# Kernel tuning notes

Hardware: AMD Instinct MI355X
Metric: run time of the kernel (lower is better)

## Reference

```python
import jax, jax.numpy as jnp
import numpy as np

V = 32          # num_variables
T = 48          # num_time_bins
D = 512         # d_model
H = 8           # num_heads
HD = D // H     # head_dim = 64
OD = 16         # observation_dim
B = 4


def setup_inputs() -> dict:
    key = jax.random.key(0)
    ks = jax.random.split(key, 20)
    s = 0.02
    inp = {
        'h': jax.random.normal(ks[0], (B, T, V, D), jnp.float32),
        'observation_state': jax.random.normal(ks[1], (B, T, V, 2), jnp.float32),
        'Wq': jax.random.normal(ks[2], (D, D), jnp.float32) * s,
        'bq': jnp.zeros((D,), jnp.float32),
        'Wk': jax.random.normal(ks[3], (D, D), jnp.float32) * s,
        'bk': jnp.zeros((D,), jnp.float32),
        'Wv': jax.random.normal(ks[4], (D, D), jnp.float32) * s,
        'bv': jnp.zeros((D,), jnp.float32),
        'Wo': jax.random.normal(ks[5], (D, D), jnp.float32) * s,
        'bo': jnp.zeros((D,), jnp.float32),
        'Woq': jax.random.normal(ks[6], (2, H * OD), jnp.float32) * 0.5,
        'boq': jnp.zeros((H * OD,), jnp.float32),
        'Wok': jax.random.normal(ks[7], (2, H * OD), jnp.float32) * 0.5,
        'bok': jnp.zeros((H * OD,), jnp.float32),
        'variable_bias': jax.random.normal(ks[8], (H, V, V), jnp.float32) * 0.01,
        'relative_time_bias': jax.random.normal(ks[9], (H, 2 * T - 1), jnp.float32) * 0.01,
    }
    return inp


def reference(h, observation_state, Wq, bq, Wk, bk, Wv, bv, Wo, bo,
              Woq, boq, Wok, bok, variable_bias, relative_time_bias):
    N = T * V
    scale = 1.0 / np.sqrt(HD)
    obs_scale = 1.0 / np.sqrt(OD)

    # static index buffers (constants)
    flat_var_ids = jnp.tile(jnp.arange(V), T)                       # [N]
    flat_time_ids = jnp.repeat(jnp.arange(T), V)                    # [N]
    rel_index = flat_time_ids[:, None] - flat_time_ids[None, :] + (T - 1)  # [N,N]

    fh = h.reshape(B, N, D)
    fo = observation_state.reshape(B, N, 2)

    def heads(x, nh, hd):
        return x.reshape(B, N, nh, hd).transpose(0, 2, 1, 3)  # [B,H,N,hd]

    q = heads(fh @ Wq + bq, H, HD)
    k = heads(fh @ Wk + bk, H, HD)
    v = heads(fh @ Wv + bv, H, HD)
    oq = heads(fo @ Woq + boq, H, OD)
    ok = heads(fo @ Wok + bok, H, OD)

    content = jnp.einsum('bhnd,bhmd->bhnm', q, k) * scale
    obs = jnp.einsum('bhnd,bhmd->bhnm', oq, ok) * obs_scale
    var_scores = variable_bias[:, flat_var_ids[:, None], flat_var_ids[None, :]]  # [H,N,N]
    time_scores = relative_time_bias[:, rel_index]                                # [H,N,N]

    scores = content + obs + var_scores[None] + time_scores[None]
    attn = jax.nn.softmax(scores, axis=-1)  # dropout off (inference)
    out = jnp.einsum('bhnm,bhmd->bhnd', attn, v)
    out = out.transpose(0, 2, 1, 3).reshape(B, N, D)
    out = out @ Wo + bo
    return out.reshape(B, T, V, D)
```

## Files before the change

### kernel.cpp

```cpp
#include <hip/hip_runtime.h>
#include <math.h>

typedef __bf16 bf16x8 __attribute__((ext_vector_type(8)));
typedef float f32x4 __attribute__((ext_vector_type(4)));

#define NB 4
#define NT 48
#define NV 32
#define ND 512
#define NH 8
#define NN 1536
#define NBN 6144
#define L2E 1.44269504f

#define GLOAD_LDS(g, l) \
    __builtin_amdgcn_global_load_lds( \
        (const __attribute__((address_space(1))) void*)(g), \
        (__attribute__((address_space(3))) void*)(l), 16, 0, 0)

__global__ __launch_bounds__(256) void prep(
    const float* __restrict__ h, const float* __restrict__ obs,
    const float* __restrict__ Wq, const float* __restrict__ Wk,
    const float* __restrict__ Wv, const float* __restrict__ Wo,
    const float* __restrict__ bq, const float* __restrict__ bk,
    const float* __restrict__ bv,
    const float* __restrict__ Wok, const float* __restrict__ bok,
    __bf16* __restrict__ h_bf, __bf16* __restrict__ WcatT,
    __bf16* __restrict__ WoT, float* __restrict__ biascat,
    __bf16* __restrict__ kx)
{
    __shared__ float ts[64][68];
    const int tid = threadIdx.x;
    const int bx = blockIdx.x;
    if (bx < 1536) {
        int t = bx * 256 + tid;
        const float4* src = (const float4*)h + (size_t)t * 2;
        float4 a = src[0], b = src[1];
        __bf16 r[8] = {(__bf16)a.x, (__bf16)a.y, (__bf16)a.z, (__bf16)a.w,
                       (__bf16)b.x, (__bf16)b.y, (__bf16)b.z, (__bf16)b.w};
        *(uint4*)(h_bf + (size_t)t * 8) = *(uint4*)r;
    } else if (bx < 1792) {
        int bw = bx - 1536;
        const int p = bw >> 6, tile = bw & 63;
        const int k0 = (tile >> 3) * 64, c0 = (tile & 7) * 64;
        const float* W = (p == 0) ? Wq : (p == 1) ? Wk : (p == 2) ? Wv : Wo;
        const float scale = (p == 0) ? 0.125f * L2E : 1.0f;
        #pragma unroll
        for (int i = 0; i < 4; i++) {
            int r = (tid >> 4) + i * 16;
            float4 v = *(const float4*)(W + (size_t)(k0 + r) * 512 + c0 + (tid & 15) * 4);
            *(float4*)&ts[r][(tid & 15) * 4] = v;
        }
        __syncthreads();
        __bf16 tmp[16];
        #pragma unroll
        for (int j = 0; j < 16; j++)
            tmp[j] = (__bf16)(ts[(tid & 3) * 16 + j][tid >> 2] * scale);
        int crow = c0 + (tid >> 2);
        __bf16* dst = (p < 3)
            ? WcatT + ((size_t)(p * 512 + crow)) * 512 + k0 + (tid & 3) * 16
            : WoT   + ((size_t)crow) * 512 + k0 + (tid & 3) * 16;
        *(uint4*)dst = *(uint4*)tmp;
        *(uint4*)(dst + 8) = *(uint4*)(tmp + 8);
        if (p < 3 && k0 == 0 && tid < 64) {
            const float* bb = (p == 0) ? bq : (p == 1) ? bk : bv;
            biascat[p * 512 + c0 + tid] = bb[c0 + tid] * scale;
        }
    } else {
        int t = (bx - 1792) * 256 + tid;
        int row = t >> 1, half = t & 1;
        __bf16* dst = kx + (size_t)row * 96 + 64 + half * 16;
        if (half == 0) {
            int bh = row / NN, n = row - bh * NN;
            int b = bh >> 3, hh = bh & 7;
            size_t bn = (size_t)b * NN + n;
            float o0 = obs[bn * 2], o1 = obs[bn * 2 + 1];
            int f = hh * 16;
            __bf16 tmp[16];
            #pragma unroll
            for (int j = 0; j < 16; j++)
                tmp[j] = (__bf16)(o0 * Wok[f + j] + o1 * Wok[128 + f + j] + bok[f + j]);
            *(uint4*)dst       = *(uint4*)tmp;
            *(uint4*)(dst + 8) = *(uint4*)(tmp + 8);
        } else {
            uint4 z = {0, 0, 0, 0};
            *(uint4*)dst       = z;
            *(uint4*)(dst + 8) = z;
        }
    }
}

__global__ __launch_bounds__(256) void kvprep(const __bf16* __restrict__ qkv,
                                              __bf16* __restrict__ kx,
                                              __bf16* __restrict__ vt)
{
    __shared__ __bf16 ts[64][72];
    const int tid = threadIdx.x;
    const int nt = blockIdx.x, bh = blockIdx.y;
    const int b = bh >> 3, h = bh & 7;
    const int n0 = nt * 64;
    {
        const __bf16* src = qkv + (size_t)(b * NN + n0 + (tid >> 2)) * 1536
                                + 512 + h * 64 + (tid & 3) * 16;
        __bf16* dst = kx + ((size_t)bh * NN + n0 + (tid >> 2)) * 96 + (tid & 3) * 16;
        *(uint4*)dst       = *(const uint4*)src;
        *(uint4*)(dst + 8) = *(const uint4*)(src + 8);
    }
    const __bf16* src = qkv + ((size_t)(b * NN + n0 + (tid >> 2))) * 1536
                            + 1024 + h * 64 + (tid & 3) * 16;
    *(uint4*)&ts[tid >> 2][(tid & 3) * 16]     = *(const uint4*)src;
    *(uint4*)&ts[tid >> 2][(tid & 3) * 16 + 8] = *(const uint4*)(src + 8);
    __syncthreads();
    __bf16 tmp[16];
    #pragma unroll
    for (int j = 0; j < 16; j++)
        tmp[j] = ts[(tid & 3) * 16 + j][tid >> 2];
    __bf16* dst = vt + ((size_t)bh * 64 + (tid >> 2)) * 1536 + n0 + (tid & 3) * 16;
    *(uint4*)dst       = *(uint4*)tmp;
    *(uint4*)(dst + 8) = *(uint4*)(tmp + 8);
}

template<int TM, bool BF16OUT>
__global__ __launch_bounds__(256) void gemm_mfma(
    const __bf16* __restrict__ A, const __bf16* __restrict__ Bt,
    const float* __restrict__ bias, float* __restrict__ Cf,
    __bf16* __restrict__ Cbf, int Ncol)
{
    constexpr int MT = TM / 32;
    __shared__ __align__(16) __bf16 As[TM][32];
    __shared__ __align__(16) __bf16 Bs[128][32];
    const int tid = threadIdx.x;
    const int w = tid >> 6, lane = tid & 63;
    const int quad = lane >> 4, l16 = lane & 15;
    const int wm = w >> 1, wn = w & 1;
    const int n0 = blockIdx.x * 128, m0 = blockIdx.y * TM;

    const int sm = tid >> 2;
    const int sk = ((tid & 3) ^ ((sm >> 1) & 3)) * 8;
    const __bf16* aptr = A  + (size_t)(m0 + sm) * 512 + sk;
    const __bf16* bptr = Bt + (size_t)(n0 + sm) * 512 + sk;
    __bf16* lA = (__bf16*)As + tid * 8;
    __bf16* lB = (__bf16*)Bs + tid * 8;

    f32x4 zero4 = {0.f, 0.f, 0.f, 0.f};
    f32x4 acc[MT][4];
    #pragma unroll
    for (int i = 0; i < MT; i++)
        #pragma unroll
        for (int j = 0; j < 4; j++) acc[i][j] = zero4;

    for (int kt = 0; kt < 512; kt += 32) {
        __syncthreads();
        GLOAD_LDS(aptr + kt, lA);
        if (TM == 128) GLOAD_LDS(aptr + 64 * 512 + kt, lA + 2048);
        GLOAD_LDS(bptr + kt, lB);
        GLOAD_LDS(bptr + 64 * 512 + kt, lB + 2048);
        __syncthreads();
        bf16x8 af[MT], bfr[4];
        #pragma unroll
        for (int mt = 0; mt < MT; mt++) {
            int rr = wm * (TM / 2) + mt * 16 + l16;
            af[mt] = *(const bf16x8*)&As[rr][(quad ^ ((rr >> 1) & 3)) * 8];
        }
        #pragma unroll
        for (int nt = 0; nt < 4; nt++) {
            int rr = wn * 64 + nt * 16 + l16;
            bfr[nt] = *(const bf16x8*)&Bs[rr][(quad ^ ((rr >> 1) & 3)) * 8];
        }
        #pragma unroll
        for (int mt = 0; mt < MT; mt++)
            #pragma unroll
            for (int nt = 0; nt < 4; nt++)
                acc[mt][nt] = __builtin_amdgcn_mfma_f32_16x16x32_bf16(
                    af[mt], bfr[nt], acc[mt][nt], 0, 0, 0);
    }

    #pragma unroll
    for (int mt = 0; mt < MT; mt++) {
        #pragma unroll
        for (int nt = 0; nt < 4; nt++) {
            int c = n0 + wn * 64 + nt * 16 + l16;
            float bia = bias[c];
            #pragma unroll
            for (int r = 0; r < 4; r++) {
                int row = m0 + wm * (TM / 2) + mt * 16 + quad * 4 + r;
                float val = acc[mt][nt][r] + bia;
                if (BF16OUT) Cbf[(size_t)row * Ncol + c] = (__bf16)val;
                else         Cf[(size_t)row * Ncol + c] = val;
            }
        }
    }
}

__global__ __launch_bounds__(256) void attn_mfma(
    const __bf16* __restrict__ qkv, const __bf16* __restrict__ kx,
    const __bf16* __restrict__ vt, const float* __restrict__ obs,
    const float* __restrict__ Woq, const float* __restrict__ boq,
    const float* __restrict__ varb, const float* __restrict__ rtb,
    __bf16* __restrict__ aout)
{
    __shared__ __align__(16) __bf16 Ks[64][128];
    __shared__ __align__(16) __bf16 Vs[64][64];
    __shared__ __align__(16) __bf16 Ps[64][64];
    __shared__ float rts[96];

    const int tid = threadIdx.x;
    const int w = tid >> 6, lane = tid & 63;
    const int quad = lane >> 4, l16 = lane & 15;
    const int qt = blockIdx.x, bh = blockIdx.y;
    const int b = bh >> 3, h = bh & 7;
    const int n0 = qt * 64;

    if (tid < 95) rts[tid] = rtb[h * 95 + tid] * L2E;

    const size_t qrow = (size_t)(b * NN + n0 + w * 16 + l16);
    bf16x8 aq[3];
    aq[0] = *(const bf16x8*)(qkv + qrow * 1536 + h * 64 + quad * 8);
    aq[1] = *(const bf16x8*)(qkv + qrow * 1536 + h * 64 + 32 + quad * 8);
    {
        uint4 a2u = {0u, 0u, 0u, 0u};
        if (quad < 2) {
            float o0 = obs[qrow * 2], o1 = obs[qrow * 2 + 1];
            int f = h * 16 + quad * 8;
            const float sc = 0.25f * L2E;
            __bf16 tmp[8];
            #pragma unroll
            for (int j = 0; j < 8; j++)
                tmp[j] = (__bf16)(sc * (o0 * Woq[f + j] + o1 * Woq[128 + f + j]
                                        + boq[f + j]));
            a2u = *(uint4*)tmp;
        }
        aq[2] = *(bf16x8*)&a2u;
    }

    float vb0[4], vb1[4];
    #pragma unroll
    for (int r = 0; r < 4; r++) {
        int rm = (w * 16 + quad * 4 + r) & 31;
        vb0[r] = varb[h * 1024 + rm * 32 + l16] * L2E;
        vb1[r] = varb[h * 1024 + rm * 32 + 16 + l16] * L2E;
    }
    const int tn = 2 * qt + (w >> 1);

    const int ck = (tid & 15) ^ ((tid >> 4) & 7);
    const __bf16* kbase = kx + (size_t)bh * NN * 96 + ck * 8;
    const int cv = (tid & 7) ^ ((tid >> 3) & 7);
    const __bf16* vbase = vt + (size_t)bh * 64 * 1536 + cv * 8;

    f32x4 zero4 = {0.f, 0.f, 0.f, 0.f};
    f32x4 o[4];
    float lpart[4];
    #pragma unroll
    for (int i = 0; i < 4; i++) { o[i] = zero4; lpart[i] = 0.f; }

    char* ldsK = (char*)Ks;
    char* ldsV = (char*)Vs;

    for (int mt = 0; mt < 24; mt++) {
        const int m0 = mt * 64;
        __syncthreads();
        #pragma unroll
        for (int i = 0; i < 4; i++) {
            int row = i * 16 + (tid >> 4);
            GLOAD_LDS(kbase + (size_t)(m0 + row) * 96, ldsK + i * 4096 + tid * 16);
        }
        #pragma unroll
        for (int i = 0; i < 2; i++) {
            int row = i * 32 + (tid >> 3);
            GLOAD_LDS(vbase + (size_t)row * 1536 + m0, ldsV + i * 4096 + tid * 16);
        }
        __syncthreads();

        f32x4 sc[4];
        #pragma unroll
        for (int ct = 0; ct < 4; ct++) {
            f32x4 d = zero4;
            int row = ct * 16 + l16;
            #pragma unroll
            for (int ks = 0; ks < 3; ks++) {
                bf16x8 bf = *(const bf16x8*)((const char*)Ks + row * 256
                                + (((ks * 4 + quad) ^ (row & 7)) * 16));
                d = __builtin_amdgcn_mfma_f32_16x16x32_bf16(aq[ks], bf, d, 0, 0, 0);
            }
            sc[ct] = d;
        }
        float tb0 = rts[tn - 2 * mt + 47];
        float tb1 = rts[tn - 2 * mt + 46];
        #pragma unroll
        for (int ct = 0; ct < 4; ct++) {
            float tb = (ct & 2) ? tb1 : tb0;
            #pragma unroll
            for (int r = 0; r < 4; r++) {
                float s = sc[ct][r] + tb + ((ct & 1) ? vb1[r] : vb0[r]);
                float p = exp2f(s);
                lpart[r] += p;
                int rowp = w * 16 + quad * 4 + r;
                int pc = ((ct * 2) + (l16 >> 3)) ^ (rowp & 7);
                Ps[rowp][pc * 8 + (l16 & 7)] = (__bf16)p;
            }
        }
        #pragma unroll
        for (int ks = 0; ks < 2; ks++) {
            int rowr = w * 16 + l16;
            bf16x8 pf = *(const bf16x8*)&Ps[rowr][((ks * 4 + quad) ^ (l16 & 7)) * 8];
            #pragma unroll
            for (int dt = 0; dt < 4; dt++) {
                int rw = dt * 16 + l16;
                bf16x8 vf = *(const bf16x8*)((const char*)Vs + rw * 128
                                + (((ks * 4 + quad) ^ (rw & 7)) * 16));
                o[dt] = __builtin_amdgcn_mfma_f32_16x16x32_bf16(pf, vf, o[dt], 0, 0, 0);
            }
        }
    }

    #pragma unroll
    for (int r = 0; r < 4; r++) {
        float l = lpart[r];
        l += __shfl_xor(l, 1);
        l += __shfl_xor(l, 2);
        l += __shfl_xor(l, 4);
        l += __shfl_xor(l, 8);
        float inv = 1.0f / l;
        int n = n0 + w * 16 + quad * 4 + r;
        size_t base = ((size_t)b * NN + n) * 512 + h * 64 + l16;
        #pragma unroll
        for (int dt = 0; dt < 4; dt++)
            aout[base + dt * 16] = (__bf16)(o[dt][r] * inv);
    }
}

extern "C" void kernel_launch(void* const* d_in, const int* in_sizes, int n_in,
                              void* d_out, int out_size, void* d_ws, size_t ws_size,
                              hipStream_t stream)
{
    const float* h_   = (const float*)d_in[0];
    const float* obs  = (const float*)d_in[1];
    const float* Wq   = (const float*)d_in[2];
    const float* bq   = (const float*)d_in[3];
    const float* Wk   = (const float*)d_in[4];
    const float* bk   = (const float*)d_in[5];
    const float* Wv   = (const float*)d_in[6];
    const float* bv   = (const float*)d_in[7];
    const float* Wo   = (const float*)d_in[8];
    const float* bo   = (const float*)d_in[9];
    const float* Woq  = (const float*)d_in[10];
    const float* boq  = (const float*)d_in[11];
    const float* Wok  = (const float*)d_in[12];
    const float* bok  = (const float*)d_in[13];
    const float* varb = (const float*)d_in[14];
    const float* rtb  = (const float*)d_in[15];
    float* out = (float*)d_out;

    char* ws = (char*)d_ws;
    __bf16* h_bf    = (__bf16*)ws;                 ws += (size_t)NBN * 512 * 2;
    __bf16* qkv     = (__bf16*)ws;                 ws += (size_t)NBN * 1536 * 2;
    __bf16* kx      = (__bf16*)ws;                 ws += ((size_t)32 * NN * 96 + 64) * 2;
    __bf16* attnout = (__bf16*)ws;                 ws += (size_t)NBN * 512 * 2;
    __bf16* WcatT   = (__bf16*)ws;                 ws += (size_t)1536 * 512 * 2;
    __bf16* WoT     = (__bf16*)ws;                 ws += (size_t)512 * 512 * 2;
    float*  biascat = (float*)ws;                  ws += 1536 * 4;
    __bf16* vt      = h_bf;

    prep<<<dim3(2176), dim3(256), 0, stream>>>(
        h_, obs, Wq, Wk, Wv, Wo, bq, bk, bv, Wok, bok,
        h_bf, WcatT, WoT, biascat, kx);
    gemm_mfma<128, true><<<dim3(12, 48), dim3(256), 0, stream>>>(
        h_bf, WcatT, biascat, nullptr, qkv, 1536);
    kvprep<<<dim3(24, 32), dim3(256), 0, stream>>>(qkv, kx, vt);
    attn_mfma<<<dim3(24, 32), dim3(256), 0, stream>>>(qkv, kx, vt, obs, Woq, boq,
                                                      varb, rtb, attnout);
    gemm_mfma<64, false><<<dim3(4, 96), dim3(256), 0, stream>>>(
        attnout, WoT, bo, out, nullptr, 512);
}
```

Before: 187.5 us.

## Stage GEMM epilogue through LDS and scatter K directly into attention layout

```diff
diff --git a/kernel.cpp b/kernel.cpp
--- a/kernel.cpp
+++ b/kernel.cpp
@@ -90,8 +90,7 @@
     }
 }
 
-__global__ __launch_bounds__(256) void kvprep(const __bf16* __restrict__ qkv,
-                                              __bf16* __restrict__ kx,
+__global__ __launch_bounds__(256) void kvprep(const __bf16* __restrict__ varr,
                                               __bf16* __restrict__ vt)
 {
     __shared__ __bf16 ts[64][72];
@@ -99,15 +98,8 @@
     const int nt = blockIdx.x, bh = blockIdx.y;
     const int b = bh >> 3, h = bh & 7;
     const int n0 = nt * 64;
-    {
-        const __bf16* src = qkv + (size_t)(b * NN + n0 + (tid >> 2)) * 1536
-                                + 512 + h * 64 + (tid & 3) * 16;
-        __bf16* dst = kx + ((size_t)bh * NN + n0 + (tid >> 2)) * 96 + (tid & 3) * 16;
-        *(uint4*)dst       = *(const uint4*)src;
-        *(uint4*)(dst + 8) = *(const uint4*)(src + 8);
-    }
-    const __bf16* src = qkv + ((size_t)(b * NN + n0 + (tid >> 2))) * 1536
-                            + 1024 + h * 64 + (tid & 3) * 16;
+    const __bf16* src = varr + (size_t)(b * NN + n0 + (tid >> 2)) * 512
+                             + h * 64 + (tid & 3) * 16;
     *(uint4*)&ts[tid >> 2][(tid & 3) * 16]     = *(const uint4*)src;
     *(uint4*)&ts[tid >> 2][(tid & 3) * 16 + 8] = *(const uint4*)(src + 8);
     __syncthreads();
@@ -124,11 +116,13 @@
 __global__ __launch_bounds__(256) void gemm_mfma(
     const __bf16* __restrict__ A, const __bf16* __restrict__ Bt,
     const float* __restrict__ bias, float* __restrict__ Cf,
-    __bf16* __restrict__ Cbf, int Ncol)
+    __bf16* __restrict__ qarr, __bf16* __restrict__ kx,
+    __bf16* __restrict__ varr)
 {
     constexpr int MT = TM / 32;
-    __shared__ __align__(16) __bf16 As[TM][32];
-    __shared__ __align__(16) __bf16 Bs[128][32];
+    __shared__ __align__(16) char smem[33792];
+    __bf16 (*As)[32] = (__bf16(*)[32])smem;
+    __bf16 (*Bs)[32] = (__bf16(*)[32])(smem + TM * 64);
     const int tid = threadIdx.x;
     const int w = tid >> 6, lane = tid & 63;
     const int quad = lane >> 4, l16 = lane & 15;
@@ -175,25 +169,66 @@
                     af[mt], bfr[nt], acc[mt][nt], 0, 0, 0);
     }
 
-    #pragma unroll
-    for (int mt = 0; mt < MT; mt++) {
-        #pragma unroll
-        for (int nt = 0; nt < 4; nt++) {
-            int c = n0 + wn * 64 + nt * 16 + l16;
-            float bia = bias[c];
-            #pragma unroll
-            for (int r = 0; r < 4; r++) {
-                int row = m0 + wm * (TM / 2) + mt * 16 + quad * 4 + r;
-                float val = acc[mt][nt][r] + bia;
-                if (BF16OUT) Cbf[(size_t)row * Ncol + c] = (__bf16)val;
-                else         Cf[(size_t)row * Ncol + c] = val;
+    __syncthreads();
+    if (BF16OUT) {
+        __bf16* Cs = (__bf16*)smem;
+        #pragma unroll
+        for (int mt = 0; mt < MT; mt++)
+            #pragma unroll
+            for (int nt = 0; nt < 4; nt++) {
+                int c = n0 + wn * 64 + nt * 16 + l16;
+                float bia = bias[c];
+                int cl = wn * 64 + nt * 16 + l16;
+                #pragma unroll
+                for (int r = 0; r < 4; r++) {
+                    int rl = wm * (TM / 2) + mt * 16 + quad * 4 + r;
+                    Cs[rl * 132 + cl] = (__bf16)(acc[mt][nt][r] + bia);
+                }
             }
+        __syncthreads();
+        int rl = tid >> 1, hb = tid & 1;
+        int grow = m0 + rl;
+        int col0 = n0 + hb * 64;
+        int p = col0 >> 9, f0 = col0 & 511, hh = f0 >> 6;
+        int bidx = grow / NN, n = grow - bidx * NN;
+        __bf16* dst = (p == 0) ? qarr + (size_t)grow * 512 + f0
+                    : (p == 1) ? kx + ((size_t)(bidx * 8 + hh) * NN + n) * 96
+                               : varr + (size_t)grow * 512 + f0;
+        #pragma unroll
+        for (int j = 0; j < 8; j++) {
+            uint2 lo = *(uint2*)&Cs[rl * 132 + hb * 64 + j * 8];
+            uint2 hi = *(uint2*)&Cs[rl * 132 + hb * 64 + j * 8 + 4];
+            uint4 v = {lo.x, lo.y, hi.x, hi.y};
+            *(uint4*)(dst + j * 8) = v;
+        }
+    } else {
+        float* Csf = (float*)smem;
+        #pragma unroll
+        for (int mt = 0; mt < MT; mt++)
+            #pragma unroll
+            for (int nt = 0; nt < 4; nt++) {
+                int c = n0 + wn * 64 + nt * 16 + l16;
+                float bia = bias[c];
+                int cl = wn * 64 + nt * 16 + l16;
+                #pragma unroll
+                for (int r = 0; r < 4; r++) {
+                    int rl = wm * (TM / 2) + mt * 16 + quad * 4 + r;
+                    Csf[rl * 132 + cl] = acc[mt][nt][r] + bia;
+                }
+            }
+        __syncthreads();
+        int rl = tid >> 2, q4 = tid & 3;
+        float* dst = Cf + (size_t)(m0 + rl) * 512 + n0 + q4 * 32;
+        #pragma unroll
+        for (int j = 0; j < 8; j++) {
+            uint4 v = *(uint4*)&Csf[rl * 132 + q4 * 32 + j * 4];
+            *(uint4*)(dst + j * 4) = v;
         }
     }
 }
 
 __global__ __launch_bounds__(256) void attn_mfma(
-    const __bf16* __restrict__ qkv, const __bf16* __restrict__ kx,
+    const __bf16* __restrict__ qarr, const __bf16* __restrict__ kx,
     const __bf16* __restrict__ vt, const float* __restrict__ obs,
     const float* __restrict__ Woq, const float* __restrict__ boq,
     const float* __restrict__ varb, const float* __restrict__ rtb,
@@ -213,10 +248,11 @@
 
     if (tid < 95) rts[tid] = rtb[h * 95 + tid] * L2E;
 
-    const size_t qrow = (size_t)(b * NN + n0 + w * 16 + l16);
-    bf16x8 aq[3];
-    aq[0] = *(const bf16x8*)(qkv + qrow * 1536 + h * 64 + quad * 8);
-    aq[1] = *(const bf16x8*)(qkv + qrow * 1536 + h * 64 + 32 + quad * 8);
+    const int nl = w * 16 + l16;
+    const size_t qrow = (size_t)(b * NN + n0 + nl);
+    bf16x8 bq_[3];
+    bq_[0] = *(const bf16x8*)(qarr + qrow * 512 + h * 64 + quad * 8);
+    bq_[1] = *(const bf16x8*)(qarr + qrow * 512 + h * 64 + 32 + quad * 8);
     {
         uint4 a2u = {0u, 0u, 0u, 0u};
         if (quad < 2) {
@@ -230,16 +266,14 @@
                                         + boq[f + j]));
             a2u = *(uint4*)tmp;
         }
-        aq[2] = *(bf16x8*)&a2u;
-    }
-
-    float vb0[4], vb1[4];
-    #pragma unroll
-    for (int r = 0; r < 4; r++) {
-        int rm = (w * 16 + quad * 4 + r) & 31;
-        vb0[r] = varb[h * 1024 + rm * 32 + l16] * L2E;
-        vb1[r] = varb[h * 1024 + rm * 32 + 16 + l16] * L2E;
-    }
+        bq_[2] = *(bf16x8*)&a2u;
+    }
+
+    const int rm = (w & 1) * 16 + l16;
+    float4 vbA = *(const float4*)(varb + h * 1024 + rm * 32 + quad * 4);
+    float4 vbB = *(const float4*)(varb + h * 1024 + rm * 32 + 16 + quad * 4);
+    float vA[4] = {vbA.x * L2E, vbA.y * L2E, vbA.z * L2E, vbA.w * L2E};
+    float vB[4] = {vbB.x * L2E, vbB.y * L2E, vbB.z * L2E, vbB.w * L2E};
     const int tn = 2 * qt + (w >> 1);
 
     const int ck = (tid & 15) ^ ((tid >> 4) & 7);
@@ -247,11 +281,20 @@
     const int cv = (tid & 7) ^ ((tid >> 3) & 7);
     const __bf16* vbase = vt + (size_t)bh * 64 * 1536 + cv * 8;
 
+    int wo2[4], ro2[2];
+    #pragma unroll
+    for (int ct = 0; ct < 4; ct++)
+        wo2[ct] = (((ct * 2 + (quad >> 1)) ^ (nl & 7)) * 16) + (quad & 1) * 8;
+    #pragma unroll
+    for (int ks = 0; ks < 2; ks++)
+        ro2[ks] = ((ks * 4 + quad) ^ (nl & 7)) * 16;
+    char* psrow = (char*)Ps + nl * 128;
+
     f32x4 zero4 = {0.f, 0.f, 0.f, 0.f};
     f32x4 o[4];
-    float lpart[4];
-    #pragma unroll
-    for (int i = 0; i < 4; i++) { o[i] = zero4; lpart[i] = 0.f; }
+    float lp = 0.f;
+    #pragma unroll
+    for (int i = 0; i < 4; i++) o[i] = zero4;
 
     char* ldsK = (char*)Ks;
     char* ldsV = (char*)Vs;
@@ -278,9 +321,9 @@
             int row = ct * 16 + l16;
             #pragma unroll
             for (int ks = 0; ks < 3; ks++) {
-                bf16x8 bf = *(const bf16x8*)((const char*)Ks + row * 256
+                bf16x8 kf = *(const bf16x8*)((const char*)Ks + row * 256
                                 + (((ks * 4 + quad) ^ (row & 7)) * 16));
-                d = __builtin_amdgcn_mfma_f32_16x16x32_bf16(aq[ks], bf, d, 0, 0, 0);
+                d = __builtin_amdgcn_mfma_f32_16x16x32_bf16(kf, bq_[ks], d, 0, 0, 0);
             }
             sc[ct] = d;
         }
@@ -289,43 +332,39 @@
         #pragma unroll
         for (int ct = 0; ct < 4; ct++) {
             float tb = (ct & 2) ? tb1 : tb0;
+            const float* vv = (ct & 1) ? vB : vA;
+            __bf16 pk[4];
             #pragma unroll
             for (int r = 0; r < 4; r++) {
-                float s = sc[ct][r] + tb + ((ct & 1) ? vb1[r] : vb0[r]);
-                float p = exp2f(s);
-                lpart[r] += p;
-                int rowp = w * 16 + quad * 4 + r;
-                int pc = ((ct * 2) + (l16 >> 3)) ^ (rowp & 7);
-                Ps[rowp][pc * 8 + (l16 & 7)] = (__bf16)p;
+                float p = exp2f(sc[ct][r] + tb + vv[r]);
+                lp += p;
+                pk[r] = (__bf16)p;
             }
+            *(uint2*)(psrow + wo2[ct]) = *(uint2*)pk;
         }
         #pragma unroll
         for (int ks = 0; ks < 2; ks++) {
-            int rowr = w * 16 + l16;
-            bf16x8 pf = *(const bf16x8*)&Ps[rowr][((ks * 4 + quad) ^ (l16 & 7)) * 8];
+            bf16x8 pf = *(const bf16x8*)(psrow + ro2[ks]);
             #pragma unroll
             for (int dt = 0; dt < 4; dt++) {
                 int rw = dt * 16 + l16;
                 bf16x8 vf = *(const bf16x8*)((const char*)Vs + rw * 128
                                 + (((ks * 4 + quad) ^ (rw & 7)) * 16));
-                o[dt] = __builtin_amdgcn_mfma_f32_16x16x32_bf16(pf, vf, o[dt], 0, 0, 0);
+                o[dt] = __builtin_amdgcn_mfma_f32_16x16x32_bf16(vf, pf, o[dt], 0, 0, 0);
             }
         }
     }
 
-    #pragma unroll
-    for (int r = 0; r < 4; r++) {
-        float l = lpart[r];
-        l += __shfl_xor(l, 1);
-        l += __shfl_xor(l, 2);
-        l += __shfl_xor(l, 4);
-        l += __shfl_xor(l, 8);
-        float inv = 1.0f / l;
-        int n = n0 + w * 16 + quad * 4 + r;
-        size_t base = ((size_t)b * NN + n) * 512 + h * 64 + l16;
-        #pragma unroll
-        for (int dt = 0; dt < 4; dt++)
-            aout[base + dt * 16] = (__bf16)(o[dt][r] * inv);
+    lp += __shfl_xor(lp, 16);
+    lp += __shfl_xor(lp, 32);
+    float inv = 1.0f / lp;
+    size_t abase = ((size_t)b * NN + n0 + nl) * 512 + h * 64 + quad * 4;
+    #pragma unroll
+    for (int dt = 0; dt < 4; dt++) {
+        __bf16 ov[4];
+        #pragma unroll
+        for (int r = 0; r < 4; r++) ov[r] = (__bf16)(o[dt][r] * inv);
+        *(uint2*)(aout + abase + dt * 16) = *(uint2*)ov;
     }
 }
 
@@ -353,7 +392,8 @@
 
     char* ws = (char*)d_ws;
     __bf16* h_bf    = (__bf16*)ws;                 ws += (size_t)NBN * 512 * 2;
-    __bf16* qkv     = (__bf16*)ws;                 ws += (size_t)NBN * 1536 * 2;
+    __bf16* qarr    = (__bf16*)ws;                 ws += (size_t)NBN * 512 * 2;
+    __bf16* varr    = (__bf16*)ws;                 ws += (size_t)NBN * 512 * 2;
     __bf16* kx      = (__bf16*)ws;                 ws += ((size_t)32 * NN * 96 + 64) * 2;
     __bf16* attnout = (__bf16*)ws;                 ws += (size_t)NBN * 512 * 2;
     __bf16* WcatT   = (__bf16*)ws;                 ws += (size_t)1536 * 512 * 2;
@@ -365,10 +405,10 @@
         h_, obs, Wq, Wk, Wv, Wo, bq, bk, bv, Wok, bok,
         h_bf, WcatT, WoT, biascat, kx);
     gemm_mfma<128, true><<<dim3(12, 48), dim3(256), 0, stream>>>(
-        h_bf, WcatT, biascat, nullptr, qkv, 1536);
-    kvprep<<<dim3(24, 32), dim3(256), 0, stream>>>(qkv, kx, vt);
-    attn_mfma<<<dim3(24, 32), dim3(256), 0, stream>>>(qkv, kx, vt, obs, Woq, boq,
+        h_bf, WcatT, biascat, nullptr, qarr, kx, varr);
+    kvprep<<<dim3(24, 32), dim3(256), 0, stream>>>(varr, vt);
+    attn_mfma<<<dim3(24, 32), dim3(256), 0, stream>>>(qarr, kx, vt, obs, Woq, boq,
                                                       varb, rtb, attnout);
     gemm_mfma<64, false><<<dim3(4, 96), dim3(256), 0, stream>>>(
-        attnout, WoT, bo, out, nullptr, 512);
+        attnout, WoT, bo, out, nullptr, nullptr, nullptr);
 }
```

After: 188.6 us. Within noise of the previous version (+0.6%).
